# Kernel optimization log

Measured on AMD Instinct MI355X. Metric: run time of the kernel, lower is better.

The kernel has to match this reference:

```python
import jax, jax.numpy as jnp
import numpy as np

D_MODEL = 1024
N_HEADS = 16
D_HEAD = D_MODEL // N_HEADS


def setup_inputs() -> dict:
    key = jax.random.key(0)
    k1, k2, k3 = jax.random.split(key, 3)
    B, N = 2, 2048
    x = jax.random.normal(k1, (B, N, D_MODEL), dtype=jnp.float32)
    # torch nn.Linear(d, 3d, bias=False): y = x @ W.T ; we store W_qkv as [D, 3D]
    scale_in = 1.0 / np.sqrt(D_MODEL)
    W_qkv = jax.random.uniform(k2, (D_MODEL, 3 * D_MODEL), dtype=jnp.float32,
                               minval=-scale_in, maxval=scale_in)
    W_out = jax.random.uniform(k3, (D_MODEL, D_MODEL), dtype=jnp.float32,
                               minval=-scale_in, maxval=scale_in)
    return {"x": x, "W_qkv": W_qkv, "W_out": W_out}


def reference(x, W_qkv, W_out):
    B, N, D = x.shape
    qkv = x @ W_qkv                                    # [B, N, 3D]
    q, k, v = jnp.split(qkv, 3, axis=-1)
    # [B, N, D] -> [B, H, N, d_head]
    def heads(t):
        return t.reshape(B, N, N_HEADS, D_HEAD).transpose(0, 2, 1, 3)
    q, k, v = heads(q), heads(k), heads(v)
    scores = jnp.einsum('bhnd,bhmd->bhnm', q, k) / np.sqrt(D_HEAD)  # [B,H,N,N]
    causal_mask = jnp.triu(jnp.ones((N, N), dtype=bool), k=1)
    scores = jnp.where(causal_mask, -jnp.inf, scores)
    attn = jax.nn.softmax(scores, axis=-1)             # [B,H,N,N]
    out = jnp.einsum('bhnm,bhmd->bhnd', attn, v)       # [B,H,N,d_head]
    out = out.transpose(0, 2, 1, 3).reshape(B, N, D)
    out = out @ W_out.T if False else out @ W_out      # W_out stored [D,D], x @ W
    return out, attn
```

## Files before the change

kernel.cpp:

```cpp
#include <hip/hip_runtime.h>
#include <hip/hip_bf16.h>

typedef __bf16 bf16;
typedef __bf16 bf16x4 __attribute__((ext_vector_type(4)));
typedef __bf16 bf16x8 __attribute__((ext_vector_type(8)));
typedef float  f32x4  __attribute__((ext_vector_type(4)));

#define MFMA16(a, b, c) __builtin_amdgcn_mfma_f32_16x16x32_bf16((a), (b), (c), 0, 0, 0)

typedef const __attribute__((address_space(1))) void* gptr_t;
typedef __attribute__((address_space(3))) void* sptr_t;

__device__ __forceinline__ void load_lds16(const bf16* g, bf16* l) {
  __builtin_amdgcn_global_load_lds((gptr_t)g, (sptr_t)l, 16, 0, 0);
}

__global__ __launch_bounds__(256) void detect_dtype(const unsigned short* __restrict__ w,
                                                    int* __restrict__ flag) {
  __shared__ int cnt[256];
  int c = 0;
#pragma unroll
  for (int k = 0; k < 16; ++k) {
    unsigned short v = w[(threadIdx.x * 16 + k) * 2];
    int e = (v >> 7) & 0xFF;
    c += (e >= 90 && e <= 130) ? 1 : 0;
  }
  cnt[threadIdx.x] = c;
  __syncthreads();
  if (threadIdx.x == 0) {
    int t = 0;
    for (int i = 0; i < 256; ++i) t += cnt[i];
    *flag = (t > 2048) ? 1 : 0;
  }
}

__global__ __launch_bounds__(256) void convert_to_bf16(const void* __restrict__ in,
                                                       bf16* __restrict__ out,
                                                       const int* __restrict__ flag) {
  const int i0 = (blockIdx.x * 256 + threadIdx.x) * 8;
  if (*flag) {
    *(bf16x8*)(out + i0) = *(const bf16x8*)((const bf16*)in + i0);
  } else {
    const float* p = (const float*)in;
    float4 a = *(const float4*)(p + i0);
    float4 b = *(const float4*)(p + i0 + 4);
    bf16x8 v;
    v[0] = (bf16)a.x; v[1] = (bf16)a.y; v[2] = (bf16)a.z; v[3] = (bf16)a.w;
    v[4] = (bf16)b.x; v[5] = (bf16)b.y; v[6] = (bf16)b.z; v[7] = (bf16)b.w;
    *(bf16x8*)(out + i0) = v;
  }
}

__global__ __launch_bounds__(256) void transpose_any(const void* __restrict__ in,
                                                     bf16* __restrict__ out,
                                                     const int* __restrict__ flag,
                                                     int R, int C) {
  __shared__ bf16 t[64][65];
  const int c0 = blockIdx.x * 64, r0 = blockIdx.y * 64;
  const int tid = threadIdx.x;
  const int lc = tid & 63, lr4 = tid >> 6;
  if (*flag) {
    const bf16* p = (const bf16*)in;
#pragma unroll
    for (int i = 0; i < 16; ++i) {
      int r = i * 4 + lr4;
      t[r][lc] = p[(size_t)(r0 + r) * C + c0 + lc];
    }
  } else {
    const float* p = (const float*)in;
#pragma unroll
    for (int i = 0; i < 16; ++i) {
      int r = i * 4 + lr4;
      t[r][lc] = (bf16)p[(size_t)(r0 + r) * C + c0 + lc];
    }
  }
  __syncthreads();
#pragma unroll
  for (int i = 0; i < 16; ++i) {
    int r = i * 4 + lr4;
    out[(size_t)(c0 + r) * R + r0 + lc] = t[lc][r];
  }
}

__global__ __launch_bounds__(256) void transpose_v(const bf16* __restrict__ qkv,
                                                   bf16* __restrict__ vt) {
  __shared__ bf16 t[64][65];
  const int bh = blockIdx.y, b = bh >> 4, h = bh & 15;
  const int j0 = blockIdx.x * 64;
  const int tid = threadIdx.x;
  const int lc = tid & 63, lr4 = tid >> 6;
  const bf16* src = qkv + (size_t)b * 2048 * 3072 + 2048 + (size_t)h * 64;
#pragma unroll
  for (int i = 0; i < 16; ++i) {
    int j = i * 4 + lr4;
    t[j][lc] = src[(size_t)(j0 + j) * 3072 + lc];
  }
  __syncthreads();
  bf16* dst = vt + (size_t)bh * 64 * 2048;
#pragma unroll
  for (int i = 0; i < 16; ++i) {
    int d = i * 4 + lr4;
    dst[(size_t)d * 2048 + j0 + lc] = t[lc][d];
  }
}

template <typename CT>
__global__ __launch_bounds__(256) void gemm_bt(const bf16* __restrict__ A,
                                               const bf16* __restrict__ Bt,
                                               CT* __restrict__ C,
                                               int K, int ldc) {
  __shared__ bf16 a_lds[128 * 32];
  __shared__ bf16 b_lds[128 * 32];
  const int tid = threadIdx.x;
  const int w = tid >> 6, lane = tid & 63, l15 = lane & 15, quad = lane >> 4;
  const int wr = w >> 1, wc = w & 1;
  const int m0 = blockIdx.y * 128, n0 = blockIdx.x * 128;

  const f32x4 fz = {0.f, 0.f, 0.f, 0.f};
  f32x4 acc[4][4];
#pragma unroll
  for (int i = 0; i < 4; ++i)
#pragma unroll
    for (int j = 0; j < 4; ++j) acc[i][j] = fz;

  for (int k0 = 0; k0 < K; k0 += 32) {
#pragma unroll
    for (int i = 0; i < 2; ++i) {
      int c = tid + i * 256;
      int r = c >> 2, kk = c & 3;
      load_lds16(A + (size_t)(m0 + r) * K + k0 + kk * 8, &a_lds[c * 8]);
      load_lds16(Bt + (size_t)(n0 + r) * K + k0 + kk * 8, &b_lds[c * 8]);
    }
    __syncthreads();
    bf16x8 af[4], bfr[4];
#pragma unroll
    for (int mb = 0; mb < 4; ++mb)
      af[mb] = *(const bf16x8*)&a_lds[(wr * 64 + mb * 16 + l15) * 32 + quad * 8];
#pragma unroll
    for (int nb = 0; nb < 4; ++nb)
      bfr[nb] = *(const bf16x8*)&b_lds[(wc * 64 + nb * 16 + l15) * 32 + quad * 8];
#pragma unroll
    for (int mb = 0; mb < 4; ++mb)
#pragma unroll
      for (int nb = 0; nb < 4; ++nb)
        acc[mb][nb] = MFMA16(af[mb], bfr[nb], acc[mb][nb]);
    __syncthreads();
  }

#pragma unroll
  for (int mb = 0; mb < 4; ++mb)
#pragma unroll
    for (int nb = 0; nb < 4; ++nb) {
      int row = m0 + wr * 64 + mb * 16 + quad * 4;
      int col = n0 + wc * 64 + nb * 16 + l15;
#pragma unroll
      for (int r = 0; r < 4; ++r)
        C[(size_t)(row + r) * ldc + col] = (CT)acc[mb][nb][r];
    }
}

__device__ __forceinline__ void compute_st(const bf16* k_lds, const bf16x8 (&qf)[2][2],
                                           int l15, int quad, f32x4 (&st)[8][2]) {
  const f32x4 fz = {0.f, 0.f, 0.f, 0.f};
#pragma unroll
  for (int jb = 0; jb < 8; ++jb) {
    const int jl = jb * 16 + l15;
    const char* kb = (const char*)k_lds + jl * 128;
    const int sw = (jl & 7) << 4;
    bf16x8 kf0 = *(const bf16x8*)(kb + ((quad * 16) ^ sw));
    bf16x8 kf1 = *(const bf16x8*)(kb + ((64 + quad * 16) ^ sw));
    st[jb][0] = MFMA16(kf0, qf[0][0], fz);
    st[jb][0] = MFMA16(kf1, qf[0][1], st[jb][0]);
    st[jb][1] = MFMA16(kf0, qf[1][0], fz);
    st[jb][1] = MFMA16(kf1, qf[1][1], st[jb][1]);
  }
}

__global__ __launch_bounds__(256) void fused_attn(const bf16* __restrict__ qkv,
                                                  const bf16* __restrict__ vt,
                                                  float* __restrict__ attn,
                                                  bf16* __restrict__ o_ws) {
  __shared__ bf16 k_lds[128 * 64];
  __shared__ bf16 vt_lds[64 * 128];
  __shared__ bf16 p_lds[128 * 128];

  const int qt = blockIdx.x, bh = blockIdx.y;
  const int b = bh >> 4, h = bh & 15;
  const int tid = threadIdx.x;
  const int w = tid >> 6, lane = tid & 63, l15 = lane & 15, quad = lane >> 4;
  const int q0 = qt * 128;

  const char* qkvb = (const char*)qkv;
  const size_t kbyte0 = ((size_t)b * 2048 * 3072 + 1024 + (size_t)h * 64) * 2;
  const size_t vtbyte0 = ((size_t)bh * 64) * 2048 * 2;

  bf16x8 qf[2][2];
#pragma unroll
  for (int ib = 0; ib < 2; ++ib)
#pragma unroll
    for (int ks = 0; ks < 2; ++ks) {
      const bf16* qp = qkv + ((size_t)b * 2048 + q0 + w * 32 + ib * 16 + l15) * 3072
                       + h * 64 + ks * 32 + quad * 8;
      bf16x8 v = *(const bf16x8*)qp;
      bf16x8 sv;
#pragma unroll
      for (int u = 0; u < 8; ++u) sv[u] = (bf16)((float)v[u] * 0.125f);
      qf[ib][ks] = sv;
    }

  float m_run[2] = {-3e38f, -3e38f};
  float l_run[2] = {0.f, 0.f};

  for (int kt = 0; kt <= qt; ++kt) {
#pragma unroll
    for (int c = 0; c < 4; ++c) {
      const int L = c * 4096 + tid * 16;
      const int j = L >> 7, cb = L & 127;
      const char* src = qkvb + kbyte0 + (size_t)(kt * 128 + j) * 6144 + (cb ^ ((j & 7) << 4));
      load_lds16((const bf16*)src, (bf16*)((char*)k_lds + L));
    }
    __syncthreads();

    f32x4 st[8][2];
    compute_st(k_lds, qf, l15, quad, st);

    const bool diag = (kt == qt);
#pragma unroll
    for (int ib = 0; ib < 2; ++ib) {
      const int ig = q0 + w * 32 + ib * 16 + l15;
      float tmax = -3e38f;
#pragma unroll
      for (int jb = 0; jb < 8; ++jb)
#pragma unroll
        for (int r = 0; r < 4; ++r) {
          const int jg = kt * 128 + jb * 16 + quad * 4 + r;
          float s = st[jb][ib][r];
          if (diag && jg > ig) { s = -3e38f; st[jb][ib][r] = s; }
          tmax = fmaxf(tmax, s);
        }
      tmax = fmaxf(tmax, __shfl_xor(tmax, 16));
      tmax = fmaxf(tmax, __shfl_xor(tmax, 32));
      const float mnew = fmaxf(m_run[ib], tmax);
      float tsum = 0.f;
#pragma unroll
      for (int jb = 0; jb < 8; ++jb)
#pragma unroll
        for (int r = 0; r < 4; ++r) {
          const float s = st[jb][ib][r];
          tsum += (s > -1e38f) ? __expf(s - mnew) : 0.f;
        }
      tsum += __shfl_xor(tsum, 16);
      tsum += __shfl_xor(tsum, 32);
      l_run[ib] = l_run[ib] * __expf(m_run[ib] - mnew) + tsum;
      m_run[ib] = mnew;
    }
    __syncthreads();
  }

  const float invl[2] = {1.f / l_run[0], 1.f / l_run[1]};

  f32x4 oacc[2][4];
#pragma unroll
  for (int ib = 0; ib < 2; ++ib)
#pragma unroll
    for (int db = 0; db < 4; ++db) {
      const f32x4 fz = {0.f, 0.f, 0.f, 0.f};
      oacc[ib][db] = fz;
    }

  for (int kt = 0; kt <= qt; ++kt) {
#pragma unroll
    for (int c = 0; c < 4; ++c) {
      const int L = c * 4096 + tid * 16;
      const int j = L >> 7, cb = L & 127;
      const char* src = qkvb + kbyte0 + (size_t)(kt * 128 + j) * 6144 + (cb ^ ((j & 7) << 4));
      load_lds16((const bf16*)src, (bf16*)((char*)k_lds + L));
    }
#pragma unroll
    for (int c = 0; c < 4; ++c) {
      const int L = c * 4096 + tid * 16;
      const int d = L >> 8, cb = L & 255;
      const char* src = (const char*)vt + vtbyte0 + (size_t)d * 4096 + kt * 256 + (cb ^ ((d & 7) << 4));
      load_lds16((const bf16*)src, (bf16*)((char*)vt_lds + L));
    }
    __syncthreads();

    f32x4 st[8][2];
    compute_st(k_lds, qf, l15, quad, st);

    const bool diag = (kt == qt);
#pragma unroll
    for (int ib = 0; ib < 2; ++ib) {
      const int ig = q0 + w * 32 + ib * 16 + l15;
      const int il = w * 32 + ib * 16 + l15;
#pragma unroll
      for (int jb = 0; jb < 8; ++jb) {
        bf16x4 pk;
#pragma unroll
        for (int r = 0; r < 4; ++r) {
          const int jg = kt * 128 + jb * 16 + quad * 4 + r;
          float p = __expf(st[jb][ib][r] - m_run[ib]) * invl[ib];
          if (diag && jg > ig) p = 0.f;
          pk[r] = (bf16)p;
        }
        *(bf16x4*)((char*)p_lds + il * 256 + ((jb * 32 + quad * 8) ^ ((il & 7) << 4))) = pk;
      }
    }
    __syncthreads();

    {
      float* abase = attn + ((size_t)bh << 22) + (size_t)q0 * 2048 + kt * 128;
#pragma unroll
      for (int it = 0; it < 16; ++it) {
        const int il = it * 8 + w * 2 + (lane >> 5);
        const int jb4 = (lane & 31) * 8;
        bf16x4 pv = *(const bf16x4*)((char*)p_lds + il * 256 + (jb4 ^ ((il & 7) << 4)));
        float4 f = {(float)pv[0], (float)pv[1], (float)pv[2], (float)pv[3]};
        *(float4*)(abase + (size_t)il * 2048 + (lane & 31) * 4) = f;
      }
    }

#pragma unroll
    for (int js = 0; js < 4; ++js) {
      bf16x8 pa[2], vb[4];
#pragma unroll
      for (int ib = 0; ib < 2; ++ib) {
        const int il = w * 32 + ib * 16 + l15;
        pa[ib] = *(const bf16x8*)((char*)p_lds + il * 256 + ((js * 64 + quad * 16) ^ ((il & 7) << 4)));
      }
#pragma unroll
      for (int db = 0; db < 4; ++db) {
        const int dl = db * 16 + l15;
        vb[db] = *(const bf16x8*)((char*)vt_lds + dl * 256 + ((js * 64 + quad * 16) ^ ((dl & 7) << 4)));
      }
#pragma unroll
      for (int ib = 0; ib < 2; ++ib)
#pragma unroll
        for (int db = 0; db < 4; ++db)
          oacc[ib][db] = MFMA16(pa[ib], vb[db], oacc[ib][db]);
    }
    __syncthreads();
  }

  for (int kt = qt + 1; kt < 16; ++kt) {
    float* abase = attn + ((size_t)bh << 22) + (size_t)q0 * 2048 + kt * 128;
    const float4 z4 = {0.f, 0.f, 0.f, 0.f};
#pragma unroll
    for (int it = 0; it < 16; ++it) {
      const int il = it * 8 + w * 2 + (lane >> 5);
      *(float4*)(abase + (size_t)il * 2048 + (lane & 31) * 4) = z4;
    }
  }

#pragma unroll
  for (int ib = 0; ib < 2; ++ib)
#pragma unroll
    for (int db = 0; db < 4; ++db)
#pragma unroll
      for (int r = 0; r < 4; ++r) {
        const int ig = q0 + w * 32 + ib * 16 + quad * 4 + r;
        const int dg = h * 64 + db * 16 + l15;
        o_ws[((size_t)b * 2048 + ig) * 1024 + dg] = (bf16)oacc[ib][db][r];
      }
}

extern "C" void kernel_launch(void* const* d_in, const int* in_sizes, int n_in,
                              void* d_out, int out_size, void* d_ws, size_t ws_size,
                              hipStream_t stream) {
  const void* x_raw = d_in[0];
  const void* w_qkv = d_in[1];
  const void* w_out = d_in[2];
  float* out  = (float*)d_out;
  float* attn = out + 4194304;

  bf16* ws     = (bf16*)d_ws;
  bf16* qkv_ws = ws;
  bf16* x_bf   = ws + 12582912;
  bf16* vt_ws  = ws + 12582912;
  bf16* woT    = ws + 12582912;
  bf16* wqkvT  = ws + 16777216;
  bf16* o_ws   = ws + 16777216;
  int*  flag   = (int*)(ws + 20971520);

  detect_dtype<<<1, 256, 0, stream>>>((const unsigned short*)w_qkv, flag);
  convert_to_bf16<<<2048, 256, 0, stream>>>(x_raw, x_bf, flag);
  transpose_any<<<dim3(48, 16), 256, 0, stream>>>(w_qkv, wqkvT, flag, 1024, 3072);
  gemm_bt<bf16><<<dim3(24, 32), 256, 0, stream>>>(x_bf, wqkvT, qkv_ws, 1024, 3072);
  transpose_v<<<dim3(32, 32), 256, 0, stream>>>(qkv_ws, vt_ws);
  fused_attn<<<dim3(16, 32), 256, 0, stream>>>(qkv_ws, vt_ws, attn, o_ws);
  transpose_any<<<dim3(16, 16), 256, 0, stream>>>(w_out, woT, flag, 1024, 1024);
  gemm_bt<float><<<dim3(8, 32), 256, 0, stream>>>(o_ws, woT, out, 1024, 1024);
}
```

Measured before the change: 756.8 us.

## Double-buffer K tiles in fused attention, remap query-tile order, raise MFMA priority

Result: faster. 694.7 us (-8.2%).

```diff
diff --git a/kernel.cpp b/kernel.cpp
--- a/kernel.cpp
+++ b/kernel.cpp
@@ -162,6 +162,7 @@
 __device__ __forceinline__ void compute_st(const bf16* k_lds, const bf16x8 (&qf)[2][2],
                                            int l15, int quad, f32x4 (&st)[8][2]) {
   const f32x4 fz = {0.f, 0.f, 0.f, 0.f};
+  __builtin_amdgcn_s_setprio(1);
 #pragma unroll
   for (int jb = 0; jb < 8; ++jb) {
     const int jl = jb * 16 + l15;
@@ -174,18 +175,20 @@
     st[jb][1] = MFMA16(kf0, qf[1][0], fz);
     st[jb][1] = MFMA16(kf1, qf[1][1], st[jb][1]);
   }
+  __builtin_amdgcn_s_setprio(0);
 }
 
 __global__ __launch_bounds__(256) void fused_attn(const bf16* __restrict__ qkv,
                                                   const bf16* __restrict__ vt,
                                                   float* __restrict__ attn,
                                                   bf16* __restrict__ o_ws) {
-  __shared__ bf16 k_lds[128 * 64];
+  __shared__ bf16 k_lds[2][128 * 64];
   __shared__ bf16 vt_lds[64 * 128];
   __shared__ bf16 p_lds[128 * 128];
 
-  const int qt = blockIdx.x, bh = blockIdx.y;
+  const int bh = blockIdx.y;
   const int b = bh >> 4, h = bh & 15;
+  const int qt = (bh & 16) ? (15 - (int)blockIdx.x) : (int)blockIdx.x;
   const int tid = threadIdx.x;
   const int w = tid >> 6, lane = tid & 63, l15 = lane & 15, quad = lane >> 4;
   const int q0 = qt * 128;
@@ -211,18 +214,32 @@
   float m_run[2] = {-3e38f, -3e38f};
   float l_run[2] = {0.f, 0.f};
 
-  for (int kt = 0; kt <= qt; ++kt) {
+  auto stage_k = [&](int kt, int buf) {
 #pragma unroll
     for (int c = 0; c < 4; ++c) {
       const int L = c * 4096 + tid * 16;
       const int j = L >> 7, cb = L & 127;
       const char* src = qkvb + kbyte0 + (size_t)(kt * 128 + j) * 6144 + (cb ^ ((j & 7) << 4));
-      load_lds16((const bf16*)src, (bf16*)((char*)k_lds + L));
-    }
-    __syncthreads();
+      load_lds16((const bf16*)src, (bf16*)((char*)k_lds[buf] + L));
+    }
+  };
+  auto stage_v = [&](int kt) {
+#pragma unroll
+    for (int c = 0; c < 4; ++c) {
+      const int L = c * 4096 + tid * 16;
+      const int d = L >> 8, cb = L & 255;
+      const char* src = (const char*)vt + vtbyte0 + (size_t)d * 4096 + kt * 256 + (cb ^ ((d & 7) << 4));
+      load_lds16((const bf16*)src, (bf16*)((char*)vt_lds + L));
+    }
+  };
+
+  stage_k(0, 0);
+  __syncthreads();
+  for (int kt = 0; kt <= qt; ++kt) {
+    if (kt < qt) stage_k(kt + 1, (kt + 1) & 1);
 
     f32x4 st[8][2];
-    compute_st(k_lds, qf, l15, quad, st);
+    compute_st(k_lds[kt & 1], qf, l15, quad, st);
 
     const bool diag = (kt == qt);
 #pragma unroll
@@ -268,25 +285,14 @@
       oacc[ib][db] = fz;
     }
 
+  stage_k(0, 0);
+  __syncthreads();
   for (int kt = 0; kt <= qt; ++kt) {
-#pragma unroll
-    for (int c = 0; c < 4; ++c) {
-      const int L = c * 4096 + tid * 16;
-      const int j = L >> 7, cb = L & 127;
-      const char* src = qkvb + kbyte0 + (size_t)(kt * 128 + j) * 6144 + (cb ^ ((j & 7) << 4));
-      load_lds16((const bf16*)src, (bf16*)((char*)k_lds + L));
-    }
-#pragma unroll
-    for (int c = 0; c < 4; ++c) {
-      const int L = c * 4096 + tid * 16;
-      const int d = L >> 8, cb = L & 255;
-      const char* src = (const char*)vt + vtbyte0 + (size_t)d * 4096 + kt * 256 + (cb ^ ((d & 7) << 4));
-      load_lds16((const bf16*)src, (bf16*)((char*)vt_lds + L));
-    }
-    __syncthreads();
+    if (kt < qt) stage_k(kt + 1, (kt + 1) & 1);
+    stage_v(kt);
 
     f32x4 st[8][2];
-    compute_st(k_lds, qf, l15, quad, st);
+    compute_st(k_lds[kt & 1], qf, l15, quad, st);
 
     const bool diag = (kt == qt);
 #pragma unroll
@@ -320,6 +326,7 @@
       }
     }
 
+    __builtin_amdgcn_s_setprio(1);
 #pragma unroll
     for (int js = 0; js < 4; ++js) {
       bf16x8 pa[2], vb[4];
@@ -339,6 +346,7 @@
         for (int db = 0; db < 4; ++db)
           oacc[ib][db] = MFMA16(pa[ib], vb[db], oacc[ib][db]);
     }
+    __builtin_amdgcn_s_setprio(0);
     __syncthreads();
   }
 
```
